# Performance work log

Measured on AMD Instinct MI355X. Metric: run time of the kernel, lower is better.

Reference implementation:

```python
import jax, jax.numpy as jnp
import numpy as np

B, S, D, O, E, R, TOP_K = 4, 1024, 1024, 1024, 8, 16, 2
SCALING = 32.0 / 16.0  # lora_alpha / r
NEG_INF = -1e9  # stand-in for float('-inf'); exp underflows to 0 identically after softmax shift


def setup_inputs() -> dict:
    key = jax.random.key(0)
    ks = jax.random.split(key, 6)
    return {
        "x": jax.random.normal(ks[0], (B, S, D), jnp.float32),
        "base_w": jax.random.normal(ks[1], (O, D), jnp.float32) * 0.02,
        "base_b": jnp.zeros((O,), jnp.float32),
        "lora_A": jax.random.normal(ks[2], (E, D, R), jnp.float32) * 0.02,
        "lora_B": jax.random.normal(ks[3], (E, R, O), jnp.float32) * 0.02,
        "router_w": jax.random.normal(ks[4], (E, D), jnp.float32) * 0.02,
        "router_b": jnp.zeros((E,), jnp.float32),
    }


def reference(x, base_w, base_b, lora_A, lora_B, router_w, router_b):
    # base layer: F.linear(x, W, b)
    result = jnp.einsum('bsd,od->bso', x, base_w) + base_b
    # per-expert LoRA: ax = x @ A_e, bax = ax @ B_e
    ax = jnp.einsum('bsd,edr->bser', x, lora_A)        # [B,S,E,R]
    bax = jnp.einsum('bser,ero->bseo', ax, lora_B)     # [B,S,E,O]
    # linear router logits
    logits = jnp.einsum('bsd,ed->bse', x, router_w) + router_b  # [B,S,E]
    # top-k routing: mask logits below the k-th largest to -inf
    kth = jax.lax.top_k(logits, TOP_K)[0][..., -1:]
    masked = jnp.where(logits < kth, NEG_INF, logits)
    expert_weights = jax.nn.softmax(masked, axis=-1)   # [B,S,E]
    # combine experts, scale, add to base output
    return result + SCALING * jnp.einsum('bse,bseo->bso', expert_weights, bax)
```

## Files before the change

kernel.cpp:

```cpp
#include <hip/hip_runtime.h>
#include <cmath>

#define M_TOK 4096
#define KD    1024
#define KEXT  1152
#define NOUT  1024
#define ERDIM 128
#define SCALING 2.0f

typedef short bf16x8 __attribute__((ext_vector_type(8)));
typedef float f32x4  __attribute__((ext_vector_type(4)));

__device__ __forceinline__ ushort f2bf(float f) {
    union { float f; unsigned u; } v; v.f = f;
    unsigned r = v.u + 0x7fffu + ((v.u >> 16) & 1u);
    return (ushort)(r >> 16);
}
__device__ __forceinline__ float b2f(ushort u) {
    union { unsigned u; float f; } v; v.u = ((unsigned)u) << 16;
    return v.f;
}

typedef const unsigned int __attribute__((address_space(1)))* gas_ptr;
typedef unsigned int __attribute__((address_space(3)))* las_ptr;
__device__ __forceinline__ void gld_lds16(const ushort* g, ushort* l) {
    __builtin_amdgcn_global_load_lds((gas_ptr)g, (las_ptr)l, 16, 0, 0);
}


__global__ __launch_bounds__(256) void prep_router(
    const float* __restrict__ x, const float* __restrict__ rw,
    const float* __restrict__ rb, const float* __restrict__ base_w,
    const float* __restrict__ lora_A, const float* __restrict__ lora_B,
    ushort* __restrict__ Aext, ushort* __restrict__ Bpack,
    ushort* __restrict__ LATpack, float* __restrict__ wgt)
{
    const int tid = threadIdx.x;
    if (blockIdx.x >= 4096) {
        int tix = (blockIdx.x - 4096) * 256 + tid;
        ushort v[8];
        if (tix < 147456) {
            const int lane = tix & 63;
            const int tile = tix >> 6;
            const int kc = tile % 36, ot = tile / 36;
            const int o  = ot * 16 + (lane & 15);
            const int c0 = kc * 32 + (lane >> 4) * 8;
            if (c0 < KD) {
                const float4* src = (const float4*)(base_w + (size_t)o * KD + c0);
                float4 f0 = src[0], f1 = src[1];
                v[0]=f2bf(f0.x); v[1]=f2bf(f0.y); v[2]=f2bf(f0.z); v[3]=f2bf(f0.w);
                v[4]=f2bf(f1.x); v[5]=f2bf(f1.y); v[6]=f2bf(f1.z); v[7]=f2bf(f1.w);
            } else {
                #pragma unroll
                for (int t = 0; t < 8; t++)
                    v[t] = f2bf(lora_B[(size_t)(c0 + t - KD) * NOUT + o]);
            }
            ushort* dst = Bpack + (size_t)tix * 8;
            ((ushort4*)dst)[0] = *(ushort4*)&v[0];
            ((ushort4*)dst)[1] = *(ushort4*)&v[4];
        } else {
            const int tix2 = tix - 147456;
            const int lane = tix2 & 63;
            const int tile = tix2 >> 6;
            const int kc = tile & 31, nt = tile >> 5;
            const int er = nt * 16 + (lane & 15);
            const int d0 = kc * 32 + (lane >> 4) * 8;
            const int e = er >> 4, r = er & 15;
            #pragma unroll
            for (int t = 0; t < 8; t++)
                v[t] = f2bf(lora_A[((size_t)e * KD + d0 + t) * 16 + r]);
            ushort* dst = LATpack + (size_t)tix2 * 8;
            ((ushort4*)dst)[0] = *(ushort4*)&v[0];
            ((ushort4*)dst)[1] = *(ushort4*)&v[4];
        }
        return;
    }
    const int t = blockIdx.x;
    const float4 xv = ((const float4*)(x + (size_t)t * KD))[tid];

    ushort4 xb;
    xb.x = f2bf(xv.x); xb.y = f2bf(xv.y); xb.z = f2bf(xv.z); xb.w = f2bf(xv.w);
    ((ushort4*)(Aext + (size_t)t * KEXT))[tid] = xb;

    double p[8];
    #pragma unroll
    for (int e = 0; e < 8; e++) {
        const float4 wv = ((const float4*)(rw + (size_t)e * KD))[tid];
        p[e] = (double)(xv.x * wv.x) + (double)(xv.y * wv.y) +
               (double)(xv.z * wv.z) + (double)(xv.w * wv.w);
    }

    const int wave = tid >> 6, lane = tid & 63;
    double q0, q1, q2, q3, r0, r1, s;
    {   const bool b = lane & 1;
        double s0 = b ? p[0] : p[1];
        double s1 = b ? p[2] : p[3];
        double s2 = b ? p[4] : p[5];
        double s3 = b ? p[6] : p[7];
        q0 = (b ? p[1] : p[0]) + __shfl_xor(s0, 1);
        q1 = (b ? p[3] : p[2]) + __shfl_xor(s1, 1);
        q2 = (b ? p[5] : p[4]) + __shfl_xor(s2, 1);
        q3 = (b ? p[7] : p[6]) + __shfl_xor(s3, 1);
    }
    {   const bool b = (lane >> 1) & 1;
        double s0 = b ? q0 : q1;
        double s1 = b ? q2 : q3;
        r0 = (b ? q1 : q0) + __shfl_xor(s0, 2);
        r1 = (b ? q3 : q2) + __shfl_xor(s1, 2);
    }
    {   const bool b = (lane >> 2) & 1;
        double s0 = b ? r0 : r1;
        s = (b ? r1 : r0) + __shfl_xor(s0, 4);
    }
    s += __shfl_xor(s, 8);
    s += __shfl_xor(s, 16);
    s += __shfl_xor(s, 32);

    __shared__ double red[4][8];
    __shared__ float  lg[8];
    if (lane < 8) red[wave][lane] = s;
    __syncthreads();
    if (tid < 8) {
        double sum = red[0][tid] + red[1][tid] + red[2][tid] + red[3][tid]
                   + (double)rb[tid];
        lg[tid] = (float)sum;
    }
    __syncthreads();
    if (tid < 8) {
        float my = lg[tid];
        float m1 = -INFINITY, m2 = -INFINITY;
        #pragma unroll
        for (int i = 0; i < 8; i++) {
            float v = lg[i];
            if (v > m1) { m2 = m1; m1 = v; }
            else if (v > m2) { m2 = v; }
        }
        float denom = 0.f;
        #pragma unroll
        for (int i = 0; i < 8; i++)
            if (lg[i] >= m2) denom += expf(lg[i] - m1);
        float w = (my >= m2) ? expf(my - m1) / denom : 0.f;
        wgt[t * 8 + tid] = SCALING * w;
    }
}

__global__ __launch_bounds__(256) void gemm_main(
    const ushort* __restrict__ A, const ushort* __restrict__ Bp,
    float* __restrict__ C, const float* __restrict__ bias)
{
    __shared__ __attribute__((aligned(16))) ushort As[2][128 * 64];

    const int tid  = threadIdx.x;
    const int wave = tid >> 6;
    const int lane = tid & 63;
    const int m0  = blockIdx.x * 128;
    const int ntb = blockIdx.y * 4;

    const int srow = tid >> 3;
    const int scol = ((tid & 7) ^ (srow & 7)) * 8;
    const ushort* aP = A + (size_t)(m0 + srow) * KEXT + scol;

    const int wr = wave * 32;
    const int fm = lane & 15;
    const int q  = lane >> 4;
    const int rx = fm & 7;

    const ushort* bBase = Bp + (size_t)lane * 8;

    f32x4 acc[2][4] = {};

    auto stageA = [&](int buf, int kk) {
        ushort* d = &As[buf][tid * 8];
        #pragma unroll
        for (int p = 0; p < 4; p++)
            gld_lds16(aP + kk + (size_t)(p * 32) * KEXT, d + p * 2048);
    };
    auto loadB = [&](bf16x8 (&bf)[2][4], int ks) {
        #pragma unroll
        for (int kh = 0; kh < 2; kh++)
            #pragma unroll
            for (int ni = 0; ni < 4; ni++)
                bf[kh][ni] = *(const bf16x8*)(bBase +
                    (size_t)((ntb + ni) * 36 + ks * 2 + kh) * 512);
    };

    bf16x8 bfc[2][4], bfn[2][4];
    stageA(0, 0);
    loadB(bfc, 0);

    for (int ks = 0; ks < 18; ++ks) {
        __syncthreads();
        if (ks + 1 < 18) {
            loadB(bfn, ks + 1);
            stageA((ks + 1) & 1, (ks + 1) * 64);
        }
        const ushort* as = &As[ks & 1][0];
        bf16x8 af[2][2];
        #pragma unroll
        for (int kh = 0; kh < 2; kh++) {
            const int sg = ((kh * 4 + q) ^ rx) * 8;
            #pragma unroll
            for (int i = 0; i < 2; i++)
                af[kh][i] = *(const bf16x8*)&as[(wr + i * 16 + fm) * 64 + sg];
        }
        #pragma unroll
        for (int kh = 0; kh < 2; kh++)
            #pragma unroll
            for (int mi = 0; mi < 2; mi++)
                #pragma unroll
                for (int ni = 0; ni < 4; ni++)
                    acc[mi][ni] = __builtin_amdgcn_mfma_f32_16x16x32_bf16(
                        af[kh][mi], bfc[kh][ni], acc[mi][ni], 0, 0, 0);
        #pragma unroll
        for (int kh = 0; kh < 2; kh++)
            #pragma unroll
            for (int ni = 0; ni < 4; ni++)
                bfc[kh][ni] = bfn[kh][ni];
    }

    const int rr = q * 4;
    #pragma unroll
    for (int ni = 0; ni < 4; ni++) {
        const int col = (ntb + ni) * 16 + fm;
        const float bv = bias[col];
        #pragma unroll
        for (int mi = 0; mi < 2; mi++) {
            const int row = m0 + wr + mi * 16 + rr;
            #pragma unroll
            for (int r = 0; r < 4; r++)
                C[(size_t)(row + r) * NOUT + col] = acc[mi][ni][r] + bv;
        }
    }
}

__global__ __launch_bounds__(256) void gemm_ax(
    const ushort* __restrict__ A, const ushort* __restrict__ Lp,
    ushort* __restrict__ part)
{
    __shared__ __attribute__((aligned(16))) ushort As[2][64 * 64];

    const int tid  = threadIdx.x;
    const int wave = tid >> 6;
    const int lane = tid & 63;
    const int m0  = blockIdx.x * 64;
    const int kc0 = blockIdx.z * 8;
    part += (size_t)blockIdx.z * (M_TOK * ERDIM);

    const int srow = tid >> 3;
    const int scol = ((tid & 7) ^ (srow & 7)) * 8;
    const ushort* aP = A + (size_t)(m0 + srow) * KEXT + kc0 * 32 + scol;

    const int wr = (wave >> 1) * 32;
    const int wc = (wave & 1) * 64;
    const int fm = lane & 15;
    const int q  = lane >> 4;
    const int rx = fm & 7;

    const ushort* lBase = Lp + (size_t)lane * 8;
    const int ntw = (wave & 1) * 4;

    f32x4 acc[2][4] = {};

    auto stageA = [&](int buf, int kk) {
        ushort* d = &As[buf][tid * 8];
        #pragma unroll
        for (int p = 0; p < 2; p++)
            gld_lds16(aP + kk + (size_t)(p * 32) * KEXT, d + p * 2048);
    };
    auto loadB = [&](bf16x8 (&bf)[2][4], int ks) {
        #pragma unroll
        for (int kh = 0; kh < 2; kh++)
            #pragma unroll
            for (int ni = 0; ni < 4; ni++)
                bf[kh][ni] = *(const bf16x8*)(lBase +
                    (size_t)((ntw + ni) * 32 + kc0 + ks * 2 + kh) * 512);
    };

    bf16x8 bfc[2][4], bfn[2][4];
    stageA(0, 0);
    loadB(bfc, 0);

    for (int ks = 0; ks < 4; ++ks) {
        __syncthreads();
        if (ks + 1 < 4) {
            loadB(bfn, ks + 1);
            stageA((ks + 1) & 1, (ks + 1) * 64);
        }
        const ushort* as = &As[ks & 1][0];
        bf16x8 af[2][2];
        #pragma unroll
        for (int kh = 0; kh < 2; kh++) {
            const int sg = ((kh * 4 + q) ^ rx) * 8;
            #pragma unroll
            for (int i = 0; i < 2; i++)
                af[kh][i] = *(const bf16x8*)&as[(wr + i * 16 + fm) * 64 + sg];
        }
        #pragma unroll
        for (int kh = 0; kh < 2; kh++)
            #pragma unroll
            for (int mi = 0; mi < 2; mi++)
                #pragma unroll
                for (int ni = 0; ni < 4; ni++)
                    acc[mi][ni] = __builtin_amdgcn_mfma_f32_16x16x32_bf16(
                        af[kh][mi], bfc[kh][ni], acc[mi][ni], 0, 0, 0);
        #pragma unroll
        for (int kh = 0; kh < 2; kh++)
            #pragma unroll
            for (int ni = 0; ni < 4; ni++)
                bfc[kh][ni] = bfn[kh][ni];
    }

    const int rr = q * 4;
    #pragma unroll
    for (int ni = 0; ni < 4; ni++) {
        const int col = wc + ni * 16 + fm;
        #pragma unroll
        for (int mi = 0; mi < 2; mi++) {
            const int row = m0 + wr + mi * 16 + rr;
            #pragma unroll
            for (int r = 0; r < 4; r++)
                part[(size_t)(row + r) * ERDIM + col] = f2bf(acc[mi][ni][r]);
        }
    }
}

__global__ __launch_bounds__(256) void ax_combine(
    const ushort* __restrict__ part, const float* __restrict__ wgt,
    ushort* __restrict__ Aext)
{
    int g = blockIdx.x * 256 + threadIdx.x;
    const int t = g >> 4, gr = g & 15;
    const int er0 = gr * 8;
    const int SL = M_TOK * ERDIM;
    const int base = t * ERDIM + er0;

    ushort4 p0a = *(const ushort4*)(part + base);
    ushort4 p0b = *(const ushort4*)(part + base + 4);
    ushort4 p1a = *(const ushort4*)(part + base + SL);
    ushort4 p1b = *(const ushort4*)(part + base + SL + 4);
    ushort4 p2a = *(const ushort4*)(part + base + 2 * SL);
    ushort4 p2b = *(const ushort4*)(part + base + 2 * SL + 4);
    ushort4 p3a = *(const ushort4*)(part + base + 3 * SL);
    ushort4 p3b = *(const ushort4*)(part + base + 3 * SL + 4);

    const float w = wgt[t * 8 + (er0 >> 4)];
    ushort o[8];
    o[0] = f2bf((b2f(p0a.x) + b2f(p1a.x) + b2f(p2a.x) + b2f(p3a.x)) * w);
    o[1] = f2bf((b2f(p0a.y) + b2f(p1a.y) + b2f(p2a.y) + b2f(p3a.y)) * w);
    o[2] = f2bf((b2f(p0a.z) + b2f(p1a.z) + b2f(p2a.z) + b2f(p3a.z)) * w);
    o[3] = f2bf((b2f(p0a.w) + b2f(p1a.w) + b2f(p2a.w) + b2f(p3a.w)) * w);
    o[4] = f2bf((b2f(p0b.x) + b2f(p1b.x) + b2f(p2b.x) + b2f(p3b.x)) * w);
    o[5] = f2bf((b2f(p0b.y) + b2f(p1b.y) + b2f(p2b.y) + b2f(p3b.y)) * w);
    o[6] = f2bf((b2f(p0b.z) + b2f(p1b.z) + b2f(p2b.z) + b2f(p3b.z)) * w);
    o[7] = f2bf((b2f(p0b.w) + b2f(p1b.w) + b2f(p2b.w) + b2f(p3b.w)) * w);

    ushort* dst = Aext + (size_t)t * KEXT + KD + er0;
    ((ushort4*)dst)[0] = *(ushort4*)&o[0];
    ((ushort4*)dst)[1] = *(ushort4*)&o[4];
}

extern "C" void kernel_launch(void* const* d_in, const int* in_sizes, int n_in,
                              void* d_out, int out_size, void* d_ws, size_t ws_size,
                              hipStream_t stream) {
    const float* x        = (const float*)d_in[0];
    const float* base_w   = (const float*)d_in[1];
    const float* base_b   = (const float*)d_in[2];
    const float* lora_A   = (const float*)d_in[3];
    const float* lora_B   = (const float*)d_in[4];
    const float* router_w = (const float*)d_in[5];
    const float* router_b = (const float*)d_in[6];
    float* out = (float*)d_out;

    char* ws = (char*)d_ws;
    ushort* Aext    = (ushort*)(ws);
    ushort* Bpack   = (ushort*)(ws + 9437184);
    ushort* LATpack = (ushort*)(ws + 11796480);
    float*  wgt     = (float*) (ws + 12058624);
    ushort* part    = (ushort*)(ws + 12189696);

    prep_router<<<4736, 256, 0, stream>>>(
        x, router_w, router_b, base_w, lora_A, lora_B,
        Aext, Bpack, LATpack, wgt);
    gemm_ax<<<dim3(64, 1, 4), 256, 0, stream>>>(Aext, LATpack, part);
    ax_combine<<<256, 256, 0, stream>>>(part, wgt, Aext);
    gemm_main<<<dim3(32, 16), 256, 0, stream>>>(Aext, Bpack, out, base_b);
}
```

Before: 112.2 us.

## Fuse LoRA-A GEMM with routing-weight combine, dropping split-K partials

Replaces the split-K LoRA-A projection kernel and its separate reduction kernel with one kernel. Each block computes the full K reduction over 1024 directly from global memory without LDS staging. It scales by the routing weight and writes bf16 into the extended activation columns. This removes one launch and the partial-sum round trip through global memory. In exchange there are fewer blocks (128), a longer serial K loop per block, and uncoalesced strided scalar stores.

After: 124.2 us. 10.7% more time.

```diff
diff --git a/kernel.cpp b/kernel.cpp
--- a/kernel.cpp
+++ b/kernel.cpp
@@ -15,10 +15,6 @@
     union { float f; unsigned u; } v; v.f = f;
     unsigned r = v.u + 0x7fffu + ((v.u >> 16) & 1u);
     return (ushort)(r >> 16);
-}
-__device__ __forceinline__ float b2f(ushort u) {
-    union { unsigned u; float f; } v; v.u = ((unsigned)u) << 16;
-    return v.f;
 }
 
 typedef const unsigned int __attribute__((address_space(1)))* gas_ptr;
@@ -144,6 +140,56 @@
     }
 }
 
+__global__ __launch_bounds__(256) void gemm_ax_fused(
+    ushort* __restrict__ Aext, const ushort* __restrict__ Lp,
+    const float* __restrict__ wgt)
+{
+    const int tid  = threadIdx.x;
+    const int wave = tid >> 6;
+    const int lane = tid & 63;
+    const int m0  = blockIdx.x * 64;
+    const int n0t = blockIdx.y * 4;
+    const int wr  = (wave >> 1) * 32;
+    const int wct = (wave & 1) * 2;
+    const int fm = lane & 15;
+    const int q  = lane >> 4;
+
+    const ushort* aP = Aext + (size_t)(m0 + wr + fm) * KEXT + q * 8;
+    const ushort* lB = Lp + (size_t)(n0t + wct) * 32 * 512 + (size_t)lane * 8;
+
+    f32x4 acc[2][2] = {};
+
+    #pragma unroll 4
+    for (int kc = 0; kc < 32; ++kc) {
+        bf16x8 af[2], bf[2];
+        af[0] = *(const bf16x8*)(aP + kc * 32);
+        af[1] = *(const bf16x8*)(aP + (size_t)16 * KEXT + kc * 32);
+        bf[0] = *(const bf16x8*)(lB + (size_t)kc * 512);
+        bf[1] = *(const bf16x8*)(lB + (size_t)(32 + kc) * 512);
+        #pragma unroll
+        for (int mi = 0; mi < 2; mi++)
+            #pragma unroll
+            for (int ni = 0; ni < 2; ni++)
+                acc[mi][ni] = __builtin_amdgcn_mfma_f32_16x16x32_bf16(
+                    af[mi], bf[ni], acc[mi][ni], 0, 0, 0);
+    }
+
+    const int rr = q * 4;
+    #pragma unroll
+    for (int ni = 0; ni < 2; ni++) {
+        const int e   = n0t + wct + ni;
+        const int col = KD + e * 16 + fm;
+        #pragma unroll
+        for (int mi = 0; mi < 2; mi++)
+            #pragma unroll
+            for (int r = 0; r < 4; r++) {
+                const int row = m0 + wr + mi * 16 + rr + r;
+                const float w = wgt[row * 8 + e];
+                Aext[(size_t)row * KEXT + col] = f2bf(acc[mi][ni][r] * w);
+            }
+    }
+}
+
 __global__ __launch_bounds__(256) void gemm_main(
     const ushort* __restrict__ A, const ushort* __restrict__ Bp,
     float* __restrict__ C, const float* __restrict__ bias)
@@ -231,132 +277,6 @@
                 C[(size_t)(row + r) * NOUT + col] = acc[mi][ni][r] + bv;
         }
     }
-}
-
-__global__ __launch_bounds__(256) void gemm_ax(
-    const ushort* __restrict__ A, const ushort* __restrict__ Lp,
-    ushort* __restrict__ part)
-{
-    __shared__ __attribute__((aligned(16))) ushort As[2][64 * 64];
-
-    const int tid  = threadIdx.x;
-    const int wave = tid >> 6;
-    const int lane = tid & 63;
-    const int m0  = blockIdx.x * 64;
-    const int kc0 = blockIdx.z * 8;
-    part += (size_t)blockIdx.z * (M_TOK * ERDIM);
-
-    const int srow = tid >> 3;
-    const int scol = ((tid & 7) ^ (srow & 7)) * 8;
-    const ushort* aP = A + (size_t)(m0 + srow) * KEXT + kc0 * 32 + scol;
-
-    const int wr = (wave >> 1) * 32;
-    const int wc = (wave & 1) * 64;
-    const int fm = lane & 15;
-    const int q  = lane >> 4;
-    const int rx = fm & 7;
-
-    const ushort* lBase = Lp + (size_t)lane * 8;
-    const int ntw = (wave & 1) * 4;
-
-    f32x4 acc[2][4] = {};
-
-    auto stageA = [&](int buf, int kk) {
-        ushort* d = &As[buf][tid * 8];
-        #pragma unroll
-        for (int p = 0; p < 2; p++)
-            gld_lds16(aP + kk + (size_t)(p * 32) * KEXT, d + p * 2048);
-    };
-    auto loadB = [&](bf16x8 (&bf)[2][4], int ks) {
-        #pragma unroll
-        for (int kh = 0; kh < 2; kh++)
-            #pragma unroll
-            for (int ni = 0; ni < 4; ni++)
-                bf[kh][ni] = *(const bf16x8*)(lBase +
-                    (size_t)((ntw + ni) * 32 + kc0 + ks * 2 + kh) * 512);
-    };
-
-    bf16x8 bfc[2][4], bfn[2][4];
-    stageA(0, 0);
-    loadB(bfc, 0);
-
-    for (int ks = 0; ks < 4; ++ks) {
-        __syncthreads();
-        if (ks + 1 < 4) {
-            loadB(bfn, ks + 1);
-            stageA((ks + 1) & 1, (ks + 1) * 64);
-        }
-        const ushort* as = &As[ks & 1][0];
-        bf16x8 af[2][2];
-        #pragma unroll
-        for (int kh = 0; kh < 2; kh++) {
-            const int sg = ((kh * 4 + q) ^ rx) * 8;
-            #pragma unroll
-            for (int i = 0; i < 2; i++)
-                af[kh][i] = *(const bf16x8*)&as[(wr + i * 16 + fm) * 64 + sg];
-        }
-        #pragma unroll
-        for (int kh = 0; kh < 2; kh++)
-            #pragma unroll
-            for (int mi = 0; mi < 2; mi++)
-                #pragma unroll
-                for (int ni = 0; ni < 4; ni++)
-                    acc[mi][ni] = __builtin_amdgcn_mfma_f32_16x16x32_bf16(
-                        af[kh][mi], bfc[kh][ni], acc[mi][ni], 0, 0, 0);
-        #pragma unroll
-        for (int kh = 0; kh < 2; kh++)
-            #pragma unroll
-            for (int ni = 0; ni < 4; ni++)
-                bfc[kh][ni] = bfn[kh][ni];
-    }
-
-    const int rr = q * 4;
-    #pragma unroll
-    for (int ni = 0; ni < 4; ni++) {
-        const int col = wc + ni * 16 + fm;
-        #pragma unroll
-        for (int mi = 0; mi < 2; mi++) {
-            const int row = m0 + wr + mi * 16 + rr;
-            #pragma unroll
-            for (int r = 0; r < 4; r++)
-                part[(size_t)(row + r) * ERDIM + col] = f2bf(acc[mi][ni][r]);
-        }
-    }
-}
-
-__global__ __launch_bounds__(256) void ax_combine(
-    const ushort* __restrict__ part, const float* __restrict__ wgt,
-    ushort* __restrict__ Aext)
-{
-    int g = blockIdx.x * 256 + threadIdx.x;
-    const int t = g >> 4, gr = g & 15;
-    const int er0 = gr * 8;
-    const int SL = M_TOK * ERDIM;
-    const int base = t * ERDIM + er0;
-
-    ushort4 p0a = *(const ushort4*)(part + base);
-    ushort4 p0b = *(const ushort4*)(part + base + 4);
-    ushort4 p1a = *(const ushort4*)(part + base + SL);
-    ushort4 p1b = *(const ushort4*)(part + base + SL + 4);
-    ushort4 p2a = *(const ushort4*)(part + base + 2 * SL);
-    ushort4 p2b = *(const ushort4*)(part + base + 2 * SL + 4);
-    ushort4 p3a = *(const ushort4*)(part + base + 3 * SL);
-    ushort4 p3b = *(const ushort4*)(part + base + 3 * SL + 4);
-
-    const float w = wgt[t * 8 + (er0 >> 4)];
-    ushort o[8];
-    o[0] = f2bf((b2f(p0a.x) + b2f(p1a.x) + b2f(p2a.x) + b2f(p3a.x)) * w);
-    o[1] = f2bf((b2f(p0a.y) + b2f(p1a.y) + b2f(p2a.y) + b2f(p3a.y)) * w);
-    o[2] = f2bf((b2f(p0a.z) + b2f(p1a.z) + b2f(p2a.z) + b2f(p3a.z)) * w);
-    o[3] = f2bf((b2f(p0a.w) + b2f(p1a.w) + b2f(p2a.w) + b2f(p3a.w)) * w);
-    o[4] = f2bf((b2f(p0b.x) + b2f(p1b.x) + b2f(p2b.x) + b2f(p3b.x)) * w);
-    o[5] = f2bf((b2f(p0b.y) + b2f(p1b.y) + b2f(p2b.y) + b2f(p3b.y)) * w);
-    o[6] = f2bf((b2f(p0b.z) + b2f(p1b.z) + b2f(p2b.z) + b2f(p3b.z)) * w);
-    o[7] = f2bf((b2f(p0b.w) + b2f(p1b.w) + b2f(p2b.w) + b2f(p3b.w)) * w);
-
-    ushort* dst = Aext + (size_t)t * KEXT + KD + er0;
-    ((ushort4*)dst)[0] = *(ushort4*)&o[0];
-    ((ushort4*)dst)[1] = *(ushort4*)&o[4];
 }
 
 extern "C" void kernel_launch(void* const* d_in, const int* in_sizes, int n_in,
@@ -376,12 +296,10 @@
     ushort* Bpack   = (ushort*)(ws + 9437184);
     ushort* LATpack = (ushort*)(ws + 11796480);
     float*  wgt     = (float*) (ws + 12058624);
-    ushort* part    = (ushort*)(ws + 12189696);
 
     prep_router<<<4736, 256, 0, stream>>>(
         x, router_w, router_b, base_w, lora_A, lora_B,
         Aext, Bpack, LATpack, wgt);
-    gemm_ax<<<dim3(64, 1, 4), 256, 0, stream>>>(Aext, LATpack, part);
-    ax_combine<<<256, 256, 0, stream>>>(part, wgt, Aext);
+    gemm_ax_fused<<<dim3(64, 2), 256, 0, stream>>>(Aext, LATpack, wgt);
     gemm_main<<<dim3(32, 16), 256, 0, stream>>>(Aext, Bpack, out, base_b);
 }
```
